# Kernel tuning notes

Hardware: AMD Instinct MI355X
Metric: run time of the kernel (lower is better)

## Reference

```python
import jax, jax.numpy as jnp
import numpy as np
from jax import lax

K = 5          # kernel_size
OC = 8         # out_num_capsules
OD = 32        # out_dims


def setup_inputs() -> dict:
    key = jax.random.key(0)
    k1, k2, k3 = jax.random.split(key, 3)
    u = jax.random.normal(k1, (4, 4, 16, 128, 128), jnp.float32)            # [B, in_caps, in_dims, H, W]
    W = jax.random.normal(k2, (4, OC * OD, 16, K, K), jnp.float32) * 0.05    # per-capsule Conv2d weights (OIHW)
    bias = jax.random.normal(k3, (4, OC * OD), jnp.float32) * 0.05
    return {"u": u, "W": W, "bias": bias}


def _squash(p):
    # p: [..., out_dims]
    sq = jnp.sum(p * p, axis=-1, keepdims=True)
    return sq / (1.0 + sq) * p / jnp.sqrt(sq + 1e-9)


def reference(u, W, bias):
    B, ic, _, H, Wd = u.shape

    def conv_one(x, w, b):  # x:[B,in_dims,H,W] w:[OC*OD,in_dims,K,K]
        y = lax.conv_general_dilated(x, w, (1, 1), [(2, 2), (2, 2)],
                                     dimension_numbers=("NCHW", "OIHW", "NCHW"))
        return y + b[None, :, None, None]

    # per-capsule conv, vmapped over the in_capsule axis -> [B, ic, OC*OD, H, W]
    u_hat = jax.vmap(conv_one, in_axes=(1, 0, 0), out_axes=1)(u, W, bias)
    # -> [B, ic, H, W, OC, OD] (matches torch reshape + transpose_(1,3).transpose_(2,4))
    u_hat = u_hat.reshape(B, ic, OC, OD, H, Wd).transpose(0, 1, 4, 5, 2, 3)

    # Routing logits b start at zero. NOTE: in the source, the update `b_t_list_`
    # is a dead store (never assigned back), so b stays zero for all iterations
    # and every routing iteration produces the identical v; one effective pass.
    b_r = jnp.zeros((B, OC, H, Wd), u.dtype)
    # windowed max (torch max_pool2d pads with -inf; k=5, pad=2 == SAME)
    b_max = lax.reduce_window(b_r, -jnp.inf, lax.max, (1, 1, K, K), (1, 1, 1, 1), "SAME")
    b_max = jnp.max(b_max, axis=1, keepdims=True)                 # [B,1,H,W]
    c = jnp.exp(b_r - b_max)                                      # [B,OC,H,W]
    # conv2d_same with an all-ones (1, OC, K, K) kernel == channel-sum then SAME window-sum
    sum_c = lax.reduce_window(jnp.sum(c, axis=1, keepdims=True), 0.0, lax.add,
                              (1, 1, K, K), (1, 1, 1, 1), "SAME")  # [B,1,H,W]
    r = (c / sum_c).transpose(0, 2, 3, 1)[..., None]              # [B,H,W,OC,1]

    # r is identical for every input capsule (b==0), so fold the capsule sum
    p = jnp.sum(r[:, None] * u_hat, axis=1)                       # [B,H,W,OC,OD]
    v = _squash(p)
    # final v.transpose_(1,3).transpose_(2,4) -> [B, OC, OD, H, W]
    return v.transpose(0, 3, 4, 1, 2)
```

## Files before the change

kernel.cpp:

```cpp
#include <hip/hip_runtime.h>
#include <math.h>

typedef __attribute__((ext_vector_type(8))) __bf16 b16x8;
typedef __attribute__((ext_vector_type(4))) float f32x4;

#define GLDS(gp, lp) __builtin_amdgcn_global_load_lds(                         \
    (const __attribute__((address_space(1))) unsigned int*)(gp),               \
    (__attribute__((address_space(3))) unsigned int*)(lp), 16, 0, 0)

#define WAIT_VM2()   asm volatile("s_waitcnt vmcnt(2)" ::: "memory")
#define WAIT_VM0()   asm volatile("s_waitcnt vmcnt(0)" ::: "memory")
#define BAR()        __builtin_amdgcn_s_barrier()

__device__ __forceinline__ unsigned short f2bf(float x) {
    unsigned int v = __float_as_uint(x);
    v += 0x7fffu + ((v >> 16) & 1u);
    return (unsigned short)(v >> 16);
}

__device__ __forceinline__ float red16(float x) {
    int v;
    v = __builtin_amdgcn_update_dpp(0, __float_as_int(x), 0xB1, 0xF, 0xF, true);
    x += __int_as_float(v);
    v = __builtin_amdgcn_update_dpp(0, __float_as_int(x), 0x4E, 0xF, 0xF, true);
    x += __int_as_float(v);
    v = __builtin_amdgcn_update_dpp(0, __float_as_int(x), 0x141, 0xF, 0xF, true);
    x += __int_as_float(v);
    v = __builtin_amdgcn_update_dpp(0, __float_as_int(x), 0x140, 0xF, 0xF, true);
    x += __int_as_float(v);
    return x;
}

__global__ __launch_bounds__(256) void repack_w(
    const float* __restrict__ Wt, const float* __restrict__ bias,
    unsigned short* __restrict__ wsw, float* __restrict__ wsb) {
    int idx = blockIdx.x * 256 + threadIdx.x;
    if (idx < 409600) {
        int j    = idx & 7;
        int cgp  = (idx >> 3) & 3;
        int o    = (idx >> 5) & 255;
        int ks   = (idx >> 13) & 1;
        int tap  = idx >> 14;
        int cg   = cgp ^ ((o >> 1) & 3);
        int cin  = ks * 32 + cg * 8 + j;
        int ic = cin >> 4, id = cin & 15;
        float w = Wt[((size_t)(ic * 256 + o) * 16 + id) * 25 + tap];
        wsw[idx] = f2bf(w);
    } else if (idx < 409856) {
        int o = idx - 409600;
        float s = 0.f;
        for (int ic = 0; ic < 4; ++ic) s += bias[ic * 256 + o];
        wsb[o] = s;
    }
}

__global__ __launch_bounds__(1024, 4) void caps_mfma(
    const float* __restrict__ u, const unsigned short* __restrict__ wsw,
    const float* __restrict__ wsb, float* __restrict__ out) {

    __shared__ __align__(16) unsigned short su_sh[25600];
    __shared__ __align__(16) unsigned short sw_sh[3][16384];

    const int tid  = threadIdx.x;
    const int lane = tid & 63;
    const int wid  = tid >> 6;
    const int wm   = wid >> 2;
    const int wn   = wid & 3;
    const int col  = lane & 15;
    const int cg   = lane >> 4;
    const int ybase = wm * 4;
    const int obase = wn * 64;

    const int bx  = blockIdx.x;
    const int b   = blockIdx.y;
    const int ty0 = (bx >> 3) * 16;
    const int tx0 = (bx & 7) * 16;

    int b_elem[4];
    #pragma unroll
    for (int fr = 0; fr < 4; ++fr) {
        int o = obase + fr * 16 + col;
        int cgp = cg ^ ((o >> 1) & 3);
        b_elem[fr] = o * 32 + cgp * 8;
    }

    int coffs[5];
    #pragma unroll
    for (int kw = 0; kw < 5; ++kw) {
        int hx = col + kw;
        coffs[kw] = hx * 32 + ((cg ^ ((hx >> 1) & 3)) * 8);
    }

    f32x4 acc[4][4];
    #pragma unroll
    for (int f = 0; f < 4; ++f)
        #pragma unroll
        for (int fr = 0; fr < 4; ++fr) acc[f][fr] = (f32x4)0.f;

    auto stage_u = [&](int half) {
        const float* up = u + ((size_t)b * 64 + half * 32) * 16384;
        unsigned short* dstp = su_sh + half * 12800;
        #pragma unroll 1
        for (int i = tid; i < 12800; i += 1024) {
            int c = i / 400;
            int s = i - c * 400;
            int hy = s / 20, hx = s - hy * 20;
            int gy = ty0 - 2 + hy, gx = tx0 - 2 + hx;
            float v = 0.f;
            if ((unsigned)gy < 128u && (unsigned)gx < 128u)
                v = up[(size_t)c * 16384 + gy * 128 + gx];
            int cgp = (c >> 3) ^ ((hx >> 1) & 3);
            dstp[(hy * 20 + hx) * 32 + cgp * 8 + (c & 7)] = f2bf(v);
        }
    };

    const char* wbase = ((const char*)wsw) + wid * 2048 + lane * 16;

    auto stage_w = [&](int slot, int bufI) {
        const char* src = wbase + (size_t)slot * 32768;
        char* dst = ((char*)sw_sh) + bufI * 32768 + wid * 2048;
        GLDS(src,        dst);
        GLDS(src + 1024, dst + 1024);
    };

    stage_u(0);
    stage_u(1);
    stage_w(0, 0);
    stage_w(1, 1);
    __syncthreads();

    int bufR = 0, bufW = 2;
    #pragma unroll 1
    for (int kh = 0; kh < 5; ++kh) {
        #pragma unroll
        for (int kw = 0; kw < 5; ++kw) {
            const int t  = kh * 5 + kw;
            const int tn = (t + 2 > 24) ? 24 : t + 2;

            BAR();
            const unsigned short* swb = sw_sh[bufR];
            const unsigned short* ap  = su_sh + (ybase + kh) * 640 + coffs[kw];

            b16x8 bf[4], a[4];
            #pragma unroll
            for (int fr = 0; fr < 4; ++fr)
                bf[fr] = *reinterpret_cast<const b16x8*>(swb + b_elem[fr]);
            #pragma unroll
            for (int f = 0; f < 4; ++f)
                a[f] = *reinterpret_cast<const b16x8*>(ap + f * 640);
            stage_w(tn, bufW);

            __builtin_amdgcn_s_setprio(1);
            #pragma unroll
            for (int f = 0; f < 4; ++f)
                #pragma unroll
                for (int fr = 0; fr < 4; ++fr)
                    acc[f][fr] = __builtin_amdgcn_mfma_f32_16x16x32_bf16(
                        a[f], bf[fr], acc[f][fr], 0, 0, 0);
            __builtin_amdgcn_s_setprio(0);

            #pragma unroll
            for (int fr = 0; fr < 4; ++fr)
                bf[fr] = *reinterpret_cast<const b16x8*>(swb + 8192 + b_elem[fr]);
            #pragma unroll
            for (int f = 0; f < 4; ++f)
                a[f] = *reinterpret_cast<const b16x8*>(ap + 12800 + f * 640);

            __builtin_amdgcn_s_setprio(1);
            #pragma unroll
            for (int f = 0; f < 4; ++f)
                #pragma unroll
                for (int fr = 0; fr < 4; ++fr)
                    acc[f][fr] = __builtin_amdgcn_mfma_f32_16x16x32_bf16(
                        a[f], bf[fr], acc[f][fr], 0, 0, 0);
            __builtin_amdgcn_s_setprio(0);

            WAIT_VM2();
            bufR = (bufR == 2) ? 0 : bufR + 1;
            bufW = (bufW == 2) ? 0 : bufW + 1;
        }
    }
    WAIT_VM0();

    float bsv[4];
    #pragma unroll
    for (int fr = 0; fr < 4; ++fr) bsv[fr] = wsb[obase + fr * 16 + col];

    const int xg = lane >> 4;
    #pragma unroll
    for (int f = 0; f < 4; ++f) {
        int h = ty0 + ybase + f;
        int rows = min(h + 2, 127) - max(h - 2, 0) + 1;
        #pragma unroll
        for (int p = 0; p < 2; ++p) {
            int oc = wn * 2 + p;
            float o0[4], o1[4];
            #pragma unroll
            for (int r = 0; r < 4; ++r) {
                int w = tx0 + xg * 4 + r;
                int colsv = min(w + 2, 127) - max(w - 2, 0) + 1;
                float rs = 1.0f / (8.0f * (float)(rows * colsv));
                float p0 = (acc[f][2 * p][r] + bsv[2 * p]) * rs;
                float p1 = (acc[f][2 * p + 1][r] + bsv[2 * p + 1]) * rs;
                o0[r] = p0; o1[r] = p1;
                float sv = red16(p0 * p0 + p1 * p1);
                float scale = sv / ((1.0f + sv) * sqrtf(sv + 1e-9f));
                o0[r] *= scale; o1[r] *= scale;
            }
            size_t base = ((size_t)((b * 8 + oc) * 32) + col) * 16384
                          + (size_t)h * 128 + tx0 + xg * 4;
            float4 v0 = make_float4(o0[0], o0[1], o0[2], o0[3]);
            float4 v1 = make_float4(o1[0], o1[1], o1[2], o1[3]);
            *reinterpret_cast<float4*>(out + base) = v0;
            *reinterpret_cast<float4*>(out + base + (size_t)16 * 16384) = v1;
        }
    }
}

extern "C" void kernel_launch(void* const* d_in, const int* in_sizes, int n_in,
                              void* d_out, int out_size, void* d_ws, size_t ws_size,
                              hipStream_t stream) {
    const float* u    = (const float*)d_in[0];
    const float* Wt   = (const float*)d_in[1];
    const float* bias = (const float*)d_in[2];
    unsigned short* wsw = (unsigned short*)d_ws;
    float* wsb = (float*)((char*)d_ws + 819200);

    repack_w<<<1601, 256, 0, stream>>>(Wt, bias, wsw, wsb);
    caps_mfma<<<dim3(64, 4), 1024, 0, stream>>>(u, wsw, wsb, (float*)d_out);
}
```

Measured before the change: 67.91 us.

## Reorder conv tap loop to reuse input fragments across kh and pipeline weights deeper

Repacks the weights so the tap order is kw-major with the channel split in the middle. The main loop then walks kw, then the channel half, then kh, keeping a sliding window of 8 input fragments in registers. Each kh step loads only one new A fragment instead of four. Weight staging becomes 50 smaller units with a 4-deep LDS ring buffer and three units prefetched, which doubles the number of barriers and waits while cutting LDS reads of the input tile.

```diff
diff --git a/kernel.cpp b/kernel.cpp
--- a/kernel.cpp
+++ b/kernel.cpp
@@ -39,8 +39,11 @@
         int j    = idx & 7;
         int cgp  = (idx >> 3) & 3;
         int o    = (idx >> 5) & 255;
-        int ks   = (idx >> 13) & 1;
-        int tap  = idx >> 14;
+        int l    = idx >> 13;
+        int kh   = l % 5;
+        int ks   = (l / 5) & 1;
+        int kw   = l / 10;
+        int tap  = kh * 5 + kw;
         int cg   = cgp ^ ((o >> 1) & 3);
         int cin  = ks * 32 + cg * 8 + j;
         int ic = cin >> 4, id = cin & 15;
@@ -59,7 +62,7 @@
     const float* __restrict__ wsb, float* __restrict__ out) {
 
     __shared__ __align__(16) unsigned short su_sh[25600];
-    __shared__ __align__(16) unsigned short sw_sh[3][16384];
+    __shared__ __align__(16) unsigned short sw_sh[4][8192];
 
     const int tid  = threadIdx.x;
     const int lane = tid & 63;
@@ -114,70 +117,60 @@
         }
     };
 
-    const char* wbase = ((const char*)wsw) + wid * 2048 + lane * 16;
-
-    auto stage_w = [&](int slot, int bufI) {
-        const char* src = wbase + (size_t)slot * 32768;
-        char* dst = ((char*)sw_sh) + bufI * 32768 + wid * 2048;
-        GLDS(src,        dst);
-        GLDS(src + 1024, dst + 1024);
+    const char* wbase = ((const char*)wsw) + wid * 1024 + lane * 16;
+
+    auto stage_unit = [&](int slot, int bufI) {
+        const char* src = wbase + (size_t)slot * 16384;
+        char* dst = ((char*)sw_sh) + bufI * 16384 + wid * 1024;
+        GLDS(src, dst);
     };
 
+    stage_unit(0, 0);
+    stage_unit(1, 1);
+    stage_unit(2, 2);
     stage_u(0);
     stage_u(1);
-    stage_w(0, 0);
-    stage_w(1, 1);
     __syncthreads();
 
-    int bufR = 0, bufW = 2;
+    int l = 0;
     #pragma unroll 1
-    for (int kh = 0; kh < 5; ++kh) {
-        #pragma unroll
-        for (int kw = 0; kw < 5; ++kw) {
-            const int t  = kh * 5 + kw;
-            const int tn = (t + 2 > 24) ? 24 : t + 2;
-
-            BAR();
-            const unsigned short* swb = sw_sh[bufR];
-            const unsigned short* ap  = su_sh + (ybase + kh) * 640 + coffs[kw];
-
-            b16x8 bf[4], a[4];
+    for (int kw = 0; kw < 5; ++kw) {
+        const int coff = coffs[kw];
+        #pragma unroll 1
+        for (int ks = 0; ks < 2; ++ks) {
+            const unsigned short* apb = su_sh + ks * 12800 + ybase * 640 + coff;
+            b16x8 aw[8];
             #pragma unroll
-            for (int fr = 0; fr < 4; ++fr)
-                bf[fr] = *reinterpret_cast<const b16x8*>(swb + b_elem[fr]);
+            for (int i = 0; i < 4; ++i)
+                aw[i] = *reinterpret_cast<const b16x8*>(apb + i * 640);
+
             #pragma unroll
-            for (int f = 0; f < 4; ++f)
-                a[f] = *reinterpret_cast<const b16x8*>(ap + f * 640);
-            stage_w(tn, bufW);
-
-            __builtin_amdgcn_s_setprio(1);
-            #pragma unroll
-            for (int f = 0; f < 4; ++f)
+            for (int kh = 0; kh < 5; ++kh) {
+                const int ln = (l + 3 > 49) ? 49 : l + 3;
+
+                BAR();
+                const unsigned short* swb = sw_sh[l & 3];
+                b16x8 bf[4];
                 #pragma unroll
                 for (int fr = 0; fr < 4; ++fr)
-                    acc[f][fr] = __builtin_amdgcn_mfma_f32_16x16x32_bf16(
-                        a[f], bf[fr], acc[f][fr], 0, 0, 0);
-            __builtin_amdgcn_s_setprio(0);
-
-            #pragma unroll
-            for (int fr = 0; fr < 4; ++fr)
-                bf[fr] = *reinterpret_cast<const b16x8*>(swb + 8192 + b_elem[fr]);
-            #pragma unroll
-            for (int f = 0; f < 4; ++f)
-                a[f] = *reinterpret_cast<const b16x8*>(ap + 12800 + f * 640);
-
-            __builtin_amdgcn_s_setprio(1);
-            #pragma unroll
-            for (int f = 0; f < 4; ++f)
+                    bf[fr] = *reinterpret_cast<const b16x8*>(swb + b_elem[fr]);
+                if (kh < 4)
+                    aw[kh + 4] =
+                        *reinterpret_cast<const b16x8*>(apb + (kh + 4) * 640);
+                stage_unit(ln, (l + 3) & 3);
+
+                __builtin_amdgcn_s_setprio(1);
                 #pragma unroll
-                for (int fr = 0; fr < 4; ++fr)
-                    acc[f][fr] = __builtin_amdgcn_mfma_f32_16x16x32_bf16(
-                        a[f], bf[fr], acc[f][fr], 0, 0, 0);
-            __builtin_amdgcn_s_setprio(0);
-
-            WAIT_VM2();
-            bufR = (bufR == 2) ? 0 : bufR + 1;
-            bufW = (bufW == 2) ? 0 : bufW + 1;
+                for (int f = 0; f < 4; ++f)
+                    #pragma unroll
+                    for (int fr = 0; fr < 4; ++fr)
+                        acc[f][fr] = __builtin_amdgcn_mfma_f32_16x16x32_bf16(
+                            aw[kh + f], bf[fr], acc[f][fr], 0, 0, 0);
+                __builtin_amdgcn_s_setprio(0);
+
+                WAIT_VM2();
+                ++l;
+            }
         }
     }
     WAIT_VM0();
```

After: 66.48 us. 1.02x faster.
